# Kernel optimization log

Measured on AMD Instinct MI355X. Metric: run time of the kernel, lower is better.

## Reference

```python
import jax, jax.numpy as jnp
import numpy as np

N_NODES = 100_000
N_EDGES = 1_600_000
IN_FEAT = 128
N_HEADS = 8
OUT_FEAT = 16
HF = N_HEADS * OUT_FEAT  # 128
NEG_SLOPE = 0.2


def setup_inputs() -> dict:
    key = jax.random.key(0)
    k = jax.random.split(key, 9)
    x = jax.random.normal(k[0], (N_NODES, IN_FEAT), dtype=jnp.float32)
    src = jax.random.randint(k[1], (N_EDGES,), 0, N_NODES, dtype=jnp.int64)
    dst = jax.random.randint(k[2], (N_EDGES,), 0, N_NODES, dtype=jnp.int64)
    sv = 1.0 / np.sqrt(IN_FEAT)
    sa = 1.0 / np.sqrt(HF)
    Wv = jax.random.normal(k[3], (IN_FEAT, HF), dtype=jnp.float32) * sv
    bv = jnp.zeros((HF,), dtype=jnp.float32)
    Wq = jax.random.normal(k[4], (HF, N_HEADS), dtype=jnp.float32) * sa
    bq = jnp.zeros((N_HEADS,), dtype=jnp.float32)
    Wk = jax.random.normal(k[5], (HF, N_HEADS), dtype=jnp.float32) * sa
    bk = jnp.zeros((N_HEADS,), dtype=jnp.float32)
    return {"x": x, "src": src, "dst": dst, "Wv": Wv, "bv": bv,
            "Wq": Wq, "bq": bq, "Wk": Wk, "bk": bk}


def reference(x, src, dst, Wv, bv, Wq, bq, Wk, bk):
    # Dense projections (homogeneous graph: h_src == h_dst == h)
    h = x @ Wv + bv                       # [N, H*F]
    q = h @ Wq + bq                       # [N, H]  (query, attached via dst)
    k = h @ Wk + bk                       # [N, H]  (key, attached via src)
    u = h.reshape(N_NODES, N_HEADS, OUT_FEAT)  # [N, H, F]

    # Edge scores: u_add_v('k','q') -> e_ij = k[src] + q[dst], then leaky-relu
    e = k[src] + q[dst]                   # [E, H]
    coeff = jnp.where(e >= 0, e, NEG_SLOPE * e)

    # Segment softmax over incoming edges of each destination node
    seg_max = jax.ops.segment_max(coeff, dst, num_segments=N_NODES)   # [N, H]
    ex = jnp.exp(coeff - seg_max[dst])                                # [E, H]
    denom = jax.ops.segment_sum(ex, dst, num_segments=N_NODES)       # [N, H]
    attn = ex / denom[dst]                                           # [E, H]

    # Weighted message + scatter-sum aggregate
    m = u[src] * attn[:, :, None]                                    # [E, H, F]
    v = jax.ops.segment_sum(m, dst, num_segments=N_NODES)            # [N, H, F]

    return jnp.mean(v, axis=1)                                       # [N, F]
```

## Files before the change

kernel.cpp:

```cpp
#include <hip/hip_runtime.h>
#include <hip/hip_fp16.h>

#define NFEAT 128
#define NHEADS 8
#define OUTF 16
#define NPB 256
#define MAXNB 512
#define CAP 4736

typedef _Float16 half8 __attribute__((ext_vector_type(8)));
typedef float float4v __attribute__((ext_vector_type(4)));

__global__ __launch_bounds__(1024) void prep_bin_kernel(
    const float* __restrict__ Wv, const float* __restrict__ bv,
    const float* __restrict__ Wq, const float* __restrict__ bq,
    const float* __restrict__ Wk, const float* __restrict__ bk,
    _Float16* __restrict__ Wt, float* __restrict__ bq2, float* __restrict__ bk2,
    const int* __restrict__ src, const int* __restrict__ dst,
    int* __restrict__ tail, int* __restrict__ bin, int E, int NB)
{
    __shared__ int lcnt[MAXNB];
    __shared__ int lbase[MAXNB];
    const int t = threadIdx.x;

    if (blockIdx.x == 0) {
        for (int idx = t; idx < 2048; idx += 1024) {
            const int m  = idx >> 10;
            const int j  = (idx >> 3) & 127;
            const int hd = idx & 7;
            const float* w = m ? Wk : Wq;
            float acc = 0.f;
#pragma unroll 8
            for (int c = 0; c < NFEAT; c++) acc += Wv[j * NFEAT + c] * w[c * NHEADS + hd];
            Wt[(128 + (m << 3) + hd) * 128 + j] = (_Float16)acc;

            const int n  = idx >> 4;
            const int k0 = (idx & 15) << 3;
            half8 v;
#pragma unroll
            for (int u = 0; u < 8; u++) v[u] = (_Float16)Wv[(k0 + u) * NFEAT + n];
            *(half8*)&Wt[n * 128 + k0] = v;
        }
        if (t < 16) {
            int mm = t >> 3, hh = t & 7;
            const float* ww = mm ? Wk : Wq;
            float a = mm ? bk[hh] : bq[hh];
            for (int c = 0; c < NFEAT; c++) a += bv[c] * ww[c * NHEADS + hh];
            if (mm) bk2[hh] = a;
            else    bq2[hh] = a;
        }
        return;
    }

    const int e0 = (blockIdx.x - 1) * 8192;

    for (int i = t; i < NB; i += 1024) lcnt[i] = 0;
    __syncthreads();

    int pack[8], bkt[8], rank[8];
#pragma unroll
    for (int k = 0; k < 8; k++) {
        int e = e0 + k * 1024 + t;
        bkt[k] = -1;
        if (e < E) {
            int d = dst[e];
            pack[k] = (src[e] << 8) | (d & (NPB - 1));
            bkt[k]  = d >> 8;
            rank[k] = atomicAdd(&lcnt[bkt[k]], 1);
        }
    }
    __syncthreads();
    for (int i = t; i < NB; i += 1024)
        lbase[i] = lcnt[i] ? atomicAdd(&tail[i], lcnt[i]) : 0;
    __syncthreads();

#pragma unroll
    for (int k = 0; k < 8; k++) {
        if (bkt[k] >= 0) {
            int pos = lbase[bkt[k]] + rank[k];
            if (pos < CAP) bin[(size_t)bkt[k] * CAP + pos] = pack[k];
        }
    }
}

__global__ __launch_bounds__(1024) void build_gemm_kernel(
    const int* __restrict__ bin, const int* __restrict__ tail,
    int* __restrict__ deg, int* __restrict__ off, int* __restrict__ csr,
    const float* __restrict__ x, const _Float16* __restrict__ Wt,
    const float* __restrict__ bv, const float* __restrict__ bq2,
    const float* __restrict__ bk2, unsigned char* __restrict__ hq,
    float* __restrict__ sarr, float* __restrict__ qarr,
    float* __restrict__ karr, int N, int NB, int M)
{
    __shared__ __align__(16) unsigned char smem[144 * 136 * 2];
    const int t = threadIdx.x;

    if ((int)blockIdx.x < NB) {
        int* stail = (int*)smem;
        int* lcnt  = stail + MAXNB;
        int* lcur  = lcnt + NPB;
        int* lcsr  = lcur + NPB;

        const int b = blockIdx.x;

        for (int i = t; i < MAXNB; i += 1024) stail[i] = (i < NB) ? tail[i] : 0;
        if (t < NPB) lcnt[t] = 0;
        __syncthreads();

        for (int o = 1; o < MAXNB; o <<= 1) {
            int u = (t < MAXNB && t >= o) ? stail[t - o] : 0;
            __syncthreads();
            if (t < MAXNB) stail[t] += u;
            __syncthreads();
        }
        const int gbase = (b > 0) ? stail[b - 1] : 0;
        const int cnt = min(tail[b], CAP);
        const int n0 = b << 8;
        const int* mybin = bin + (size_t)b * CAP;

        for (int i = t; i < cnt; i += 1024) atomicAdd(&lcnt[mybin[i] & (NPB - 1)], 1);
        __syncthreads();

        if (t < NPB) lcur[t] = lcnt[t];
        __syncthreads();
        for (int o = 1; o < NPB; o <<= 1) {
            int u = (t < NPB && t >= o) ? lcur[t - o] : 0;
            __syncthreads();
            if (t < NPB) lcur[t] += u;
            __syncthreads();
        }
        if (t < NPB) {
            int excl = lcur[t] - lcnt[t];
            lcur[t] = excl;
            int node = n0 + t;
            if (node < N) {
                deg[node] = lcnt[t];
                off[node] = gbase + excl;
            }
        }
        __syncthreads();

        for (int i = t; i < cnt; i += 1024) {
            int p = mybin[i];
            int r = atomicAdd(&lcur[p & (NPB - 1)], 1);
            lcsr[r] = p >> 8;
        }
        __syncthreads();

        for (int i = t; i < cnt; i += 1024) csr[gbase + i] = lcsr[i];
        return;
    }

    typedef _Float16 swrow[136];
    swrow* sw = (swrow*)smem;
    const int bid = blockIdx.x - NB;

    {
        const uint4* Wt4 = (const uint4*)Wt;
        for (int i = t; i < 144 * 16; i += 1024) {
            int col = i >> 4, c8 = (i & 15) << 3;
            *(uint4*)&sw[col][c8] = Wt4[i];
        }
    }
    __syncthreads();

    const int wave = t >> 6, lane = t & 63;
    const int quad = lane >> 4, l16 = lane & 15;
    const int nstrips = (M + 15) >> 4;

    float bvv[8];
#pragma unroll
    for (int tl = 0; tl < 8; tl++) bvv[tl] = bv[tl * 16 + l16];
    const float qb = (l16 < 8) ? bq2[l16] : bk2[l16 - 8];

#pragma unroll
    for (int s = 0; s < 2; s++) {
        const int strip = bid * 32 + wave + s * 16;
        if (strip >= nstrips) break;
        const int row0 = strip * 16;
        const int xr = row0 + l16;
        const bool ok = (xr < M);
        const float* xp = x + (size_t)xr * NFEAT + quad * 8;

        half8 af[4];
#pragma unroll
        for (int kc = 0; kc < 4; kc++) {
            float4 f0 = make_float4(0.f, 0.f, 0.f, 0.f);
            float4 f1 = make_float4(0.f, 0.f, 0.f, 0.f);
            if (ok) {
                f0 = *(const float4*)(xp + kc * 32);
                f1 = *(const float4*)(xp + kc * 32 + 4);
            }
            half8 a;
            a[0] = (_Float16)f0.x; a[1] = (_Float16)f0.y;
            a[2] = (_Float16)f0.z; a[3] = (_Float16)f0.w;
            a[4] = (_Float16)f1.x; a[5] = (_Float16)f1.y;
            a[6] = (_Float16)f1.z; a[7] = (_Float16)f1.w;
            af[kc] = a;
        }

        float4v acc[9];
#pragma unroll
        for (int tl = 0; tl < 9; tl++) acc[tl] = (float4v){0.f, 0.f, 0.f, 0.f};

#pragma unroll
        for (int kc = 0; kc < 4; kc++) {
#pragma unroll
            for (int tl = 0; tl < 9; tl++) {
                half8 b = *(const half8*)&sw[tl * 16 + l16][kc * 32 + quad * 8];
                acc[tl] = __builtin_amdgcn_mfma_f32_16x16x32_f16(af[kc], b, acc[tl], 0, 0, 0);
            }
        }

#pragma unroll
        for (int r = 0; r < 4; r++) {
            int row = row0 + quad * 4 + r;
            if (row < M) {
                float vv[8];
                float mx = 0.f;
#pragma unroll
                for (int tl = 0; tl < 8; tl++) {
                    vv[tl] = acc[tl][r] + bvv[tl];
                    mx = fmaxf(mx, fabsf(vv[tl]));
                }
#pragma unroll
                for (int o = 1; o <= 8; o <<= 1)
                    mx = fmaxf(mx, __shfl_xor(mx, o, 64));
                const float is = (mx > 0.f) ? 127.f / mx : 0.f;
#pragma unroll
                for (int tl = 0; tl < 8; tl++) {
                    int qi = __float2int_rn(vv[tl] * is);
                    hq[(size_t)row * NFEAT + tl * 16 + l16] = (unsigned char)(signed char)qi;
                }
                if (l16 == 0) sarr[row] = mx * (1.f / 127.f);
                float qv = acc[8][r] + qb;
                if (l16 < 8) qarr[(size_t)row * NHEADS + l16] = qv;
                else         karr[(size_t)row * NHEADS + (l16 - 8)] = qv;
            }
        }
    }
}

__global__ __launch_bounds__(256, 4) void agg_kernel(
    const int* __restrict__ csr, const int* __restrict__ off,
    const int* __restrict__ deg, const float* __restrict__ karr,
    const float* __restrict__ qarr, const unsigned char* __restrict__ hq,
    const float* __restrict__ sarr, float* __restrict__ out, int nnodes)
{
    const int g = threadIdx.x >> 4;
    const int jj = threadIdx.x & 15;
    const int j = jj & 7;
    const int half = jj >> 3;
    const int d = blockIdx.x * 16 + g;
    if (d >= nnodes) return;

    const int dg = deg[d];
    const int o0 = off[d];
    const float q1 = qarr[d * NHEADS + j];
    const unsigned char* hb = hq + j * 16;
    const int sfb = (dg > 0) ? csr[o0] : 0;

    float acc[16];
#pragma unroll
    for (int i = 0; i < 16; i++) acc[i] = 0.f;
    float den = 0.f;

    for (int e0 = 0; e0 < dg; e0 += 8) {
        const int eb = e0 + half * 4;
        int4 s4 = make_int4(sfb, sfb, sfb, sfb);
        if (eb < dg) s4 = *(const int4*)(csr + o0 + eb);

        int s[4] = { s4.x, s4.y, s4.z, s4.w };
        bool vld[4];
#pragma unroll
        for (int k = 0; k < 4; k++) {
            vld[k] = (eb + k < dg);
            if (!vld[k]) s[k] = sfb;
        }

        int4 r[4];
        float kv[4], sc[4];
#pragma unroll
        for (int k = 0; k < 4; k++) {
            r[k]  = *(const int4*)(hb + (size_t)s[k] * NFEAT);
            kv[k] = karr[s[k] * NHEADS + j];
            sc[k] = sarr[s[k]];
        }

#pragma unroll
        for (int k = 0; k < 4; k++) {
            float c = kv[k] + q1;
            c = fmaxf(c, 0.2f * c);
            const float p = vld[k] ? __expf(c) * 0.0009765625f : 0.f;
            den += p;
            const float w = p * sc[k];
            const int d0 = r[k].x, d1 = r[k].y, d2 = r[k].z, d3 = r[k].w;
            acc[0]  = fmaf(w, (float)(signed char)(d0      ), acc[0]);
            acc[1]  = fmaf(w, (float)(signed char)(d0 >>  8), acc[1]);
            acc[2]  = fmaf(w, (float)(signed char)(d0 >> 16), acc[2]);
            acc[3]  = fmaf(w, (float)(d0 >> 24),              acc[3]);
            acc[4]  = fmaf(w, (float)(signed char)(d1      ), acc[4]);
            acc[5]  = fmaf(w, (float)(signed char)(d1 >>  8), acc[5]);
            acc[6]  = fmaf(w, (float)(signed char)(d1 >> 16), acc[6]);
            acc[7]  = fmaf(w, (float)(d1 >> 24),              acc[7]);
            acc[8]  = fmaf(w, (float)(signed char)(d2      ), acc[8]);
            acc[9]  = fmaf(w, (float)(signed char)(d2 >>  8), acc[9]);
            acc[10] = fmaf(w, (float)(signed char)(d2 >> 16), acc[10]);
            acc[11] = fmaf(w, (float)(d2 >> 24),              acc[11]);
            acc[12] = fmaf(w, (float)(signed char)(d3      ), acc[12]);
            acc[13] = fmaf(w, (float)(signed char)(d3 >>  8), acc[13]);
            acc[14] = fmaf(w, (float)(signed char)(d3 >> 16), acc[14]);
            acc[15] = fmaf(w, (float)(d3 >> 24),              acc[15]);
        }
    }

    den += __shfl_xor(den, 8, 64);
    const float inv = (dg > 0) ? 0.125f / den : 0.f;
    float f[16];
#pragma unroll
    for (int i = 0; i < 16; i++) f[i] = acc[i] * inv;

#pragma unroll
    for (int o = 1; o <= 8; o <<= 1)
#pragma unroll
        for (int i = 0; i < 16; i++) f[i] += __shfl_xor(f[i], o, 64);

    if (jj == 0) {
        float4* o4 = (float4*)(out + (size_t)d * OUTF);
        o4[0] = make_float4(f[0],  f[1],  f[2],  f[3]);
        o4[1] = make_float4(f[4],  f[5],  f[6],  f[7]);
        o4[2] = make_float4(f[8],  f[9],  f[10], f[11]);
        o4[3] = make_float4(f[12], f[13], f[14], f[15]);
    }
}

extern "C" void kernel_launch(void* const* d_in, const int* in_sizes, int n_in,
                              void* d_out, int out_size, void* d_ws, size_t ws_size,
                              hipStream_t stream)
{
    const float* x   = (const float*)d_in[0];
    const int*   src = (const int*)d_in[1];
    const int*   dst = (const int*)d_in[2];
    const float* Wv  = (const float*)d_in[3];
    const float* bv  = (const float*)d_in[4];
    const float* Wq  = (const float*)d_in[5];
    const float* bq  = (const float*)d_in[6];
    const float* Wk  = (const float*)d_in[7];
    const float* bk  = (const float*)d_in[8];
    float* out = (float*)d_out;

    const int N = in_sizes[0] / NFEAT;
    const int E = in_sizes[1];
    const int NB = (N + NPB - 1) / NPB;

    unsigned char* hq = (unsigned char*)d_ws;
    float* sarr = (float*)(hq + (size_t)N * NFEAT);
    float* qarr = sarr + N;
    float* karr = qarr + (size_t)N * NHEADS;
    int* deg    = (int*)(karr + (size_t)N * NHEADS);
    int* off    = deg + N;
    int* csr    = off + N;
    _Float16* Wt = (_Float16*)(csr + E);
    float* bq2  = (float*)(Wt + 144 * 128);
    float* bk2  = bq2 + NHEADS;
    int* tail   = (int*)(bk2 + NHEADS);
    int* bin    = tail + MAXNB;

    hipMemsetAsync(tail, 0, MAXNB * sizeof(int), stream);

    prep_bin_kernel<<<dim3(1 + (E + 8191) / 8192), dim3(1024), 0, stream>>>(
        Wv, bv, Wq, bq, Wk, bk, Wt, bq2, bk2, src, dst, tail, bin, E, NB);

    const int nstrips = (N + 15) / 16;
    build_gemm_kernel<<<dim3(NB + (nstrips + 31) / 32), dim3(1024), 0, stream>>>(
        bin, tail, deg, off, csr,
        x, Wt, bv, bq2, bk2, hq, sarr, qarr, karr, N, NB, N);

    agg_kernel<<<dim3((N + 15) / 16), dim3(256), 0, stream>>>(
        csr, off, deg, karr, qarr, hq, sarr, out, N);
}
```

Baseline: 203.5 us.

## Shrink build/gemm blocks to 256 threads and widen aggregation edge batches

Reduces build_gemm_kernel block size from 1024 to 256 threads, replacing the full-array prefix scan of bin tails with a per-block partial-sum reduction over preceding bins. The GEMM part now processes 8 strips per block with more blocks launched. The aggregation kernel loads 8 edges per half-group per iteration instead of 4, increasing memory-level parallelism at the cost of more registers.

```diff
diff --git a/kernel.cpp b/kernel.cpp
--- a/kernel.cpp
+++ b/kernel.cpp
@@ -83,7 +83,7 @@
     }
 }
 
-__global__ __launch_bounds__(1024) void build_gemm_kernel(
+__global__ __launch_bounds__(256) void build_gemm_kernel(
     const int* __restrict__ bin, const int* __restrict__ tail,
     int* __restrict__ deg, int* __restrict__ off, int* __restrict__ csr,
     const float* __restrict__ x, const _Float16* __restrict__ Wt,
@@ -96,40 +96,41 @@
     const int t = threadIdx.x;
 
     if ((int)blockIdx.x < NB) {
-        int* stail = (int*)smem;
-        int* lcnt  = stail + MAXNB;
-        int* lcur  = lcnt + NPB;
-        int* lcsr  = lcur + NPB;
+        int* lcnt = (int*)smem;
+        int* lcur = lcnt + NPB;
+        int* lcsr = lcur + NPB;
+        int* red  = lcsr + CAP;
 
         const int b = blockIdx.x;
 
-        for (int i = t; i < MAXNB; i += 1024) stail[i] = (i < NB) ? tail[i] : 0;
-        if (t < NPB) lcnt[t] = 0;
-        __syncthreads();
-
-        for (int o = 1; o < MAXNB; o <<= 1) {
-            int u = (t < MAXNB && t >= o) ? stail[t - o] : 0;
+        int psum = 0;
+        for (int i = t; i < b; i += 256) psum += tail[i];
+        red[t] = psum;
+        __syncthreads();
+        for (int o = 128; o > 0; o >>= 1) {
+            if (t < o) red[t] += red[t + o];
             __syncthreads();
-            if (t < MAXNB) stail[t] += u;
-            __syncthreads();
-        }
-        const int gbase = (b > 0) ? stail[b - 1] : 0;
+        }
+        const int gbase = red[0];
         const int cnt = min(tail[b], CAP);
         const int n0 = b << 8;
         const int* mybin = bin + (size_t)b * CAP;
 
-        for (int i = t; i < cnt; i += 1024) atomicAdd(&lcnt[mybin[i] & (NPB - 1)], 1);
-        __syncthreads();
-
-        if (t < NPB) lcur[t] = lcnt[t];
+        lcnt[t] = 0;
+        __syncthreads();
+
+        for (int i = t; i < cnt; i += 256) atomicAdd(&lcnt[mybin[i] & (NPB - 1)], 1);
+        __syncthreads();
+
+        lcur[t] = lcnt[t];
         __syncthreads();
         for (int o = 1; o < NPB; o <<= 1) {
-            int u = (t < NPB && t >= o) ? lcur[t - o] : 0;
+            int u = (t >= o) ? lcur[t - o] : 0;
             __syncthreads();
-            if (t < NPB) lcur[t] += u;
+            lcur[t] += u;
             __syncthreads();
         }
-        if (t < NPB) {
+        {
             int excl = lcur[t] - lcnt[t];
             lcur[t] = excl;
             int node = n0 + t;
@@ -140,14 +141,14 @@
         }
         __syncthreads();
 
-        for (int i = t; i < cnt; i += 1024) {
+        for (int i = t; i < cnt; i += 256) {
             int p = mybin[i];
             int r = atomicAdd(&lcur[p & (NPB - 1)], 1);
             lcsr[r] = p >> 8;
         }
         __syncthreads();
 
-        for (int i = t; i < cnt; i += 1024) csr[gbase + i] = lcsr[i];
+        for (int i = t; i < cnt; i += 256) csr[gbase + i] = lcsr[i];
         return;
     }
 
@@ -157,7 +158,7 @@
 
     {
         const uint4* Wt4 = (const uint4*)Wt;
-        for (int i = t; i < 144 * 16; i += 1024) {
+        for (int i = t; i < 144 * 16; i += 256) {
             int col = i >> 4, c8 = (i & 15) << 3;
             *(uint4*)&sw[col][c8] = Wt4[i];
         }
@@ -175,7 +176,7 @@
 
 #pragma unroll
     for (int s = 0; s < 2; s++) {
-        const int strip = bid * 32 + wave + s * 16;
+        const int strip = bid * 8 + wave + s * 4;
         if (strip >= nstrips) break;
         const int row0 = strip * 16;
         const int xr = row0 + l16;
@@ -265,30 +266,32 @@
     for (int i = 0; i < 16; i++) acc[i] = 0.f;
     float den = 0.f;
 
-    for (int e0 = 0; e0 < dg; e0 += 8) {
-        const int eb = e0 + half * 4;
-        int4 s4 = make_int4(sfb, sfb, sfb, sfb);
-        if (eb < dg) s4 = *(const int4*)(csr + o0 + eb);
-
-        int s[4] = { s4.x, s4.y, s4.z, s4.w };
-        bool vld[4];
-#pragma unroll
-        for (int k = 0; k < 4; k++) {
+    for (int e0 = 0; e0 < dg; e0 += 16) {
+        const int eb = e0 + half * 8;
+        int4 sa = make_int4(sfb, sfb, sfb, sfb);
+        int4 sb = sa;
+        if (eb < dg)     sa = *(const int4*)(csr + o0 + eb);
+        if (eb + 4 < dg) sb = *(const int4*)(csr + o0 + eb + 4);
+
+        int s[8] = { sa.x, sa.y, sa.z, sa.w, sb.x, sb.y, sb.z, sb.w };
+        bool vld[8];
+#pragma unroll
+        for (int k = 0; k < 8; k++) {
             vld[k] = (eb + k < dg);
             if (!vld[k]) s[k] = sfb;
         }
 
-        int4 r[4];
-        float kv[4], sc[4];
-#pragma unroll
-        for (int k = 0; k < 4; k++) {
+        int4 r[8];
+        float kv[8], sc[8];
+#pragma unroll
+        for (int k = 0; k < 8; k++) {
             r[k]  = *(const int4*)(hb + (size_t)s[k] * NFEAT);
             kv[k] = karr[s[k] * NHEADS + j];
             sc[k] = sarr[s[k]];
         }
 
 #pragma unroll
-        for (int k = 0; k < 4; k++) {
+        for (int k = 0; k < 8; k++) {
             float c = kv[k] + q1;
             c = fmaxf(c, 0.2f * c);
             const float p = vld[k] ? __expf(c) * 0.0009765625f : 0.f;
@@ -372,7 +375,7 @@
         Wv, bv, Wq, bq, Wk, bk, Wt, bq2, bk2, src, dst, tail, bin, E, NB);
 
     const int nstrips = (N + 15) / 16;
-    build_gemm_kernel<<<dim3(NB + (nstrips + 31) / 32), dim3(1024), 0, stream>>>(
+    build_gemm_kernel<<<dim3(NB + (nstrips + 7) / 8), dim3(256), 0, stream>>>(
         bin, tail, deg, off, csr,
         x, Wt, bv, bq2, bk2, hq, sarr, qarr, karr, N, NB, N);
 
```

After: 343.1 us. 68.6% more time.

## Stage bin writes in LDS sorted by bucket; use offset-uint8 quantization

Applied to the files above, without the earlier changes.

The binning kernel now does a block-wide prefix scan over bucket counts, places packed edges into shared memory sorted by bucket, then writes them to global bins in a coalesced sweep instead of scattered per-thread stores. The quantized features are stored as unsigned bytes with a +128 offset, and the aggregation kernel decodes them with cheaper unsigned extracts, subtracting the bias afterward using the summed weights. The shared-memory staging adds 64KB of LDS and several barriers per block, which may lower occupancy. The bias correction also subtracts two large quantities, which could lose some float precision.

```diff
diff --git a/kernel.cpp b/kernel.cpp
--- a/kernel.cpp
+++ b/kernel.cpp
@@ -7,6 +7,7 @@
 #define NPB 256
 #define MAXNB 512
 #define CAP 4736
+#define EPB 8192
 
 typedef _Float16 half8 __attribute__((ext_vector_type(8)));
 typedef float float4v __attribute__((ext_vector_type(4)));
@@ -20,7 +21,10 @@
     int* __restrict__ tail, int* __restrict__ bin, int E, int NB)
 {
     __shared__ int lcnt[MAXNB];
+    __shared__ int lex[MAXNB];
     __shared__ int lbase[MAXNB];
+    __shared__ int spack[EPB];
+    __shared__ int saddr[EPB];
     const int t = threadIdx.x;
 
     if (blockIdx.x == 0) {
@@ -52,7 +56,8 @@
         return;
     }
 
-    const int e0 = (blockIdx.x - 1) * 8192;
+    const int e0 = (blockIdx.x - 1) * EPB;
+    const int tot = min(EPB, E - e0);
 
     for (int i = t; i < NB; i += 1024) lcnt[i] = 0;
     __syncthreads();
@@ -70,16 +75,32 @@
         }
     }
     __syncthreads();
+
+    for (int i = t; i < MAXNB; i += 1024) lex[i] = (i < NB) ? lcnt[i] : 0;
     for (int i = t; i < NB; i += 1024)
         lbase[i] = lcnt[i] ? atomicAdd(&tail[i], lcnt[i]) : 0;
     __syncthreads();
+    for (int o = 1; o < MAXNB; o <<= 1) {
+        int u = (t < MAXNB && t >= o) ? lex[t - o] : 0;
+        __syncthreads();
+        if (t < MAXNB) lex[t] += u;
+        __syncthreads();
+    }
 
 #pragma unroll
     for (int k = 0; k < 8; k++) {
         if (bkt[k] >= 0) {
-            int pos = lbase[bkt[k]] + rank[k];
-            if (pos < CAP) bin[(size_t)bkt[k] * CAP + pos] = pack[k];
-        }
+            int pos = lex[bkt[k]] - lcnt[bkt[k]] + rank[k];
+            int gr  = lbase[bkt[k]] + rank[k];
+            spack[pos] = pack[k];
+            saddr[pos] = (gr < CAP) ? bkt[k] * CAP + gr : -1;
+        }
+    }
+    __syncthreads();
+
+    for (int i = t; i < tot; i += 1024) {
+        int a = saddr[i];
+        if (a >= 0) bin[a] = spack[i];
     }
 }
 
@@ -230,7 +251,8 @@
 #pragma unroll
                 for (int tl = 0; tl < 8; tl++) {
                     int qi = __float2int_rn(vv[tl] * is);
-                    hq[(size_t)row * NFEAT + tl * 16 + l16] = (unsigned char)(signed char)qi;
+                    hq[(size_t)row * NFEAT + tl * 16 + l16] =
+                        (unsigned char)(qi + 128);
                 }
                 if (l16 == 0) sarr[row] = mx * (1.f / 127.f);
                 float qv = acc[8][r] + qb;
@@ -264,6 +286,7 @@
 #pragma unroll
     for (int i = 0; i < 16; i++) acc[i] = 0.f;
     float den = 0.f;
+    float wsum = 0.f;
 
     for (int e0 = 0; e0 < dg; e0 += 8) {
         const int eb = e0 + half * 4;
@@ -278,11 +301,11 @@
             if (!vld[k]) s[k] = sfb;
         }
 
-        int4 r[4];
+        uint4 r[4];
         float kv[4], sc[4];
 #pragma unroll
         for (int k = 0; k < 4; k++) {
-            r[k]  = *(const int4*)(hb + (size_t)s[k] * NFEAT);
+            r[k]  = *(const uint4*)(hb + (size_t)s[k] * NFEAT);
             kv[k] = karr[s[k] * NHEADS + j];
             sc[k] = sarr[s[k]];
         }
@@ -294,31 +317,33 @@
             const float p = vld[k] ? __expf(c) * 0.0009765625f : 0.f;
             den += p;
             const float w = p * sc[k];
-            const int d0 = r[k].x, d1 = r[k].y, d2 = r[k].z, d3 = r[k].w;
-            acc[0]  = fmaf(w, (float)(signed char)(d0      ), acc[0]);
-            acc[1]  = fmaf(w, (float)(signed char)(d0 >>  8), acc[1]);
-            acc[2]  = fmaf(w, (float)(signed char)(d0 >> 16), acc[2]);
-            acc[3]  = fmaf(w, (float)(d0 >> 24),              acc[3]);
-            acc[4]  = fmaf(w, (float)(signed char)(d1      ), acc[4]);
-            acc[5]  = fmaf(w, (float)(signed char)(d1 >>  8), acc[5]);
-            acc[6]  = fmaf(w, (float)(signed char)(d1 >> 16), acc[6]);
-            acc[7]  = fmaf(w, (float)(d1 >> 24),              acc[7]);
-            acc[8]  = fmaf(w, (float)(signed char)(d2      ), acc[8]);
-            acc[9]  = fmaf(w, (float)(signed char)(d2 >>  8), acc[9]);
-            acc[10] = fmaf(w, (float)(signed char)(d2 >> 16), acc[10]);
-            acc[11] = fmaf(w, (float)(d2 >> 24),              acc[11]);
-            acc[12] = fmaf(w, (float)(signed char)(d3      ), acc[12]);
-            acc[13] = fmaf(w, (float)(signed char)(d3 >>  8), acc[13]);
-            acc[14] = fmaf(w, (float)(signed char)(d3 >> 16), acc[14]);
-            acc[15] = fmaf(w, (float)(d3 >> 24),              acc[15]);
+            wsum += w;
+            const unsigned d0 = r[k].x, d1 = r[k].y, d2 = r[k].z, d3 = r[k].w;
+            acc[0]  = fmaf(w, (float)( d0        & 0xffu), acc[0]);
+            acc[1]  = fmaf(w, (float)((d0 >>  8) & 0xffu), acc[1]);
+            acc[2]  = fmaf(w, (float)((d0 >> 16) & 0xffu), acc[2]);
+            acc[3]  = fmaf(w, (float)( d0 >> 24         ), acc[3]);
+            acc[4]  = fmaf(w, (float)( d1        & 0xffu), acc[4]);
+            acc[5]  = fmaf(w, (float)((d1 >>  8) & 0xffu), acc[5]);
+            acc[6]  = fmaf(w, (float)((d1 >> 16) & 0xffu), acc[6]);
+            acc[7]  = fmaf(w, (float)( d1 >> 24         ), acc[7]);
+            acc[8]  = fmaf(w, (float)( d2        & 0xffu), acc[8]);
+            acc[9]  = fmaf(w, (float)((d2 >>  8) & 0xffu), acc[9]);
+            acc[10] = fmaf(w, (float)((d2 >> 16) & 0xffu), acc[10]);
+            acc[11] = fmaf(w, (float)( d2 >> 24         ), acc[11]);
+            acc[12] = fmaf(w, (float)( d3        & 0xffu), acc[12]);
+            acc[13] = fmaf(w, (float)((d3 >>  8) & 0xffu), acc[13]);
+            acc[14] = fmaf(w, (float)((d3 >> 16) & 0xffu), acc[14]);
+            acc[15] = fmaf(w, (float)( d3 >> 24         ), acc[15]);
         }
     }
 
     den += __shfl_xor(den, 8, 64);
     const float inv = (dg > 0) ? 0.125f / den : 0.f;
+    const float bias = 128.f * wsum;
     float f[16];
 #pragma unroll
-    for (int i = 0; i < 16; i++) f[i] = acc[i] * inv;
+    for (int i = 0; i < 16; i++) f[i] = (acc[i] - bias) * inv;
 
 #pragma unroll
     for (int o = 1; o <= 8; o <<= 1)
@@ -368,7 +393,7 @@
 
     hipMemsetAsync(tail, 0, MAXNB * sizeof(int), stream);
 
-    prep_bin_kernel<<<dim3(1 + (E + 8191) / 8192), dim3(1024), 0, stream>>>(
+    prep_bin_kernel<<<dim3(1 + (E + EPB - 1) / EPB), dim3(1024), 0, stream>>>(
         Wv, bv, Wq, bq, Wk, bk, Wt, bq2, bk2, src, dst, tail, bin, E, NB);
 
     const int nstrips = (N + 15) / 16;
```

Result: no change. 207.4 us (+1.9%).
